# Kernel optimization log

Hardware: AMD Instinct MI355X
Metric: run time of the kernel (lower is better)

The kernel has to match this reference:

```python
import jax, jax.numpy as jnp
import numpy as np

B, S, H = 2, 2048, 2048
NH, NKV, HD = 32, 8, 64
MAXP = 4096


def _apply_rope(x, cos, sin, positions):
    # x: [b, h, s, d]; cos/sin: [max_pos, d//2]; positions: [b, s]
    c = cos[positions][:, None]  # [b,1,s,d/2]
    s_ = sin[positions][:, None]
    x1 = x[..., ::2]
    x2 = x[..., 1::2]
    rotated = jnp.stack((-x2, x1), axis=-1).reshape(x.shape)  # interleave
    c2 = jnp.concatenate([c, c], axis=-1)   # repeat(1,1,1,2) tiling
    s2 = jnp.concatenate([s_, s_], axis=-1)
    return x * c2 + rotated * s2


def setup_inputs() -> dict:
    key = jax.random.key(0)
    ks = jax.random.split(key, 10)
    hidden_states = jax.random.normal(ks[0], (B, S, H), dtype=jnp.float32)
    # RoPE tables (use real rotary tables for realism)
    inv_freq = 1.0 / (10000.0 ** (jnp.arange(0, HD, 2, dtype=jnp.float32) / HD))
    t = jnp.arange(MAXP, dtype=jnp.float32)
    freqs = jnp.outer(t, inv_freq)  # [max_pos, d/2]
    cos = jnp.cos(freqs)
    sin = jnp.sin(freqs)
    positions = jnp.broadcast_to(jnp.arange(S, dtype=jnp.int32), (B, S))
    # additive causal mask
    neg = jnp.finfo(jnp.float32).min
    mask = jnp.where(jnp.tril(jnp.ones((S, S), dtype=bool)), 0.0, neg)[None, None]
    sc = 1.0 / np.sqrt(H)
    q_w = jax.random.normal(ks[1], (NH * HD, H), dtype=jnp.float32) * sc
    q_b = jnp.zeros((NH * HD,), dtype=jnp.float32)
    k_w = jax.random.normal(ks[2], (NKV * HD, H), dtype=jnp.float32) * sc
    k_b = jnp.zeros((NKV * HD,), dtype=jnp.float32)
    v_w = jax.random.normal(ks[3], (NKV * HD, H), dtype=jnp.float32) * sc
    v_b = jnp.zeros((NKV * HD,), dtype=jnp.float32)
    o_w = jax.random.normal(ks[4], (H, NH * HD), dtype=jnp.float32) * sc
    return {"hidden_states": hidden_states, "cos": cos, "sin": sin,
            "positions": positions, "mask": mask,
            "q_w": q_w, "q_b": q_b, "k_w": k_w, "k_b": k_b,
            "v_w": v_w, "v_b": v_b, "o_w": o_w}


def reference(hidden_states, cos, sin, positions, mask, q_w, q_b, k_w, k_b, v_w, v_b, o_w):
    bsz, seq_len, _ = hidden_states.shape
    groups = NH // NKV
    q = (hidden_states @ q_w.T + q_b).reshape(bsz, seq_len, NH, HD).transpose(0, 2, 1, 3)
    k = (hidden_states @ k_w.T + k_b).reshape(bsz, seq_len, NKV, HD).transpose(0, 2, 1, 3)
    v = (hidden_states @ v_w.T + v_b).reshape(bsz, seq_len, NKV, HD).transpose(0, 2, 1, 3)
    q = _apply_rope(q, cos, sin, positions)
    k = _apply_rope(k, cos, sin, positions)
    if groups > 1:
        k = jnp.repeat(k, groups, axis=1)
        v = jnp.repeat(v, groups, axis=1)
    scale = 1.0 / np.sqrt(HD)
    attn = jnp.einsum('bhqd,bhkd->bhqk', q, k) * scale
    attn = attn + mask
    attn = jax.nn.softmax(attn.astype(jnp.float32), axis=-1).astype(q.dtype)
    out = jnp.einsum('bhqk,bhkd->bhqd', attn, v)
    out = out.transpose(0, 2, 1, 3).reshape(bsz, seq_len, NH * HD)
    return out @ o_w.T
```

## Files before the change

kernel.cpp:

```cpp
#include <hip/hip_runtime.h>
#include <hip/hip_bf16.h>

#define BB   2
#define SS   2048
#define HH   2048
#define NH   32
#define NKV  8
#define HD   64
#define NTOK (BB * SS)
#define NQKV (NH * HD + 2 * NKV * HD)
#define KOFF (NH * HD)
#define VOFF (NH * HD + NKV * HD)

#define QSC  0.1803368801111244f

typedef short  short8  __attribute__((ext_vector_type(8)));
typedef short  short4v __attribute__((ext_vector_type(4)));
typedef float  float4v __attribute__((ext_vector_type(4)));

using bf16 = __hip_bfloat16;

#define DEV static __device__ __forceinline__

DEV short8 load8(const bf16* p) { return *(const short8*)p; }
DEV short8 load8s(const short* p) { return *(const short8*)p; }

DEV short f2bfbits(float f) {
    union { bf16 h; short s; } u;
    u.h = __float2bfloat16(f);
    return u.s;
}

DEV unsigned int packbf2(float a, float b) {
    return (unsigned int)(unsigned short)f2bfbits(a)
         | ((unsigned int)(unsigned short)f2bfbits(b) << 16);
}

DEV void async16(const bf16* g, short* l) {
    __builtin_amdgcn_global_load_lds(
        (const __attribute__((address_space(1))) unsigned int*)g,
        (__attribute__((address_space(3))) unsigned int*)l, 16, 0, 0);
}

__global__ __launch_bounds__(256) void cvt_all_kernel(
    const float* __restrict__ hidden, const float* __restrict__ q_w,
    const float* __restrict__ k_w, const float* __restrict__ v_w,
    const float* __restrict__ o_w,
    bf16* __restrict__ Hb, bf16* __restrict__ Wqkv, bf16* __restrict__ Wo) {
    int blk = blockIdx.x;
    const float* src;
    bf16* dst;
    int off;
    if (blk < 8192)       { src = hidden; dst = Hb;   off = blk * 1024; }
    else if (blk < 12288) { src = q_w; dst = Wqkv;    off = (blk - 8192) * 1024; }
    else if (blk < 13312) { src = k_w; dst = Wqkv + (size_t)KOFF * HH; off = (blk - 12288) * 1024; }
    else if (blk < 14336) { src = v_w; dst = Wqkv + (size_t)VOFF * HH; off = (blk - 13312) * 1024; }
    else                  { src = o_w; dst = Wo;      off = (blk - 14336) * 1024; }
    int i = off + threadIdx.x * 4;
    float4 v = *(const float4*)(src + i);
    short4v o;
    o[0] = f2bfbits(v.x); o[1] = f2bfbits(v.y);
    o[2] = f2bfbits(v.z); o[3] = f2bfbits(v.w);
    *(short4v*)(dst + i) = o;
}
#define CVT_BLOCKS 18432

struct GemmCtx {
    const bf16 *gA, *gB;
    short *lA, *lB;
    const short *rdA, *rdB;
    int p0;
};

DEV void gemm_setup(GemmCtx& c, const bf16* A, const bf16* Bw, int K,
                    int m0, int n0, short* As, short* Bs) {
    int lane = threadIdx.x & 63, w = threadIdx.x >> 6;
    int quad = lane >> 4, tq = lane & 15;
    int srow = lane >> 3;
    int schunk = (lane & 7) ^ srow;
    c.gA = A  + (size_t)(m0 + w * 32 + srow) * K + schunk * 8;
    c.gB = Bw + (size_t)(n0 + w * 32 + srow) * K + schunk * 8;
    c.lA = As + (w * 32) * 64;
    c.lB = Bs + (w * 32) * 64;
    int mbase = (w >> 1) * 64, nbase = (w & 1) * 64;
    c.rdA = As + (mbase + tq) * 64;
    c.rdB = Bs + (nbase + tq) * 64;
    c.p0 = (quad ^ (tq & 7)) * 8;
}

DEV void gemm_mainloop(GemmCtx& c, int K, float4v acc[4][4]) {
    for (int k0 = 0; k0 < K; k0 += 64) {
        __syncthreads();
#pragma unroll
        for (int cc = 0; cc < 4; ++cc) {
            async16(c.gA + (size_t)cc * 8 * K + k0, c.lA + cc * 8 * 64);
            async16(c.gB + (size_t)cc * 8 * K + k0, c.lB + cc * 8 * 64);
        }
        __syncthreads();
#pragma unroll
        for (int kh = 0; kh < 2; ++kh) {
            int off = c.p0 ^ (kh * 32);
            short8 af[4], bfr[4];
#pragma unroll
            for (int mi = 0; mi < 4; ++mi) af[mi]  = load8s(c.rdA + mi * 16 * 64 + off);
#pragma unroll
            for (int nj = 0; nj < 4; ++nj) bfr[nj] = load8s(c.rdB + nj * 16 * 64 + off);
#pragma unroll
            for (int mi = 0; mi < 4; ++mi)
#pragma unroll
                for (int nj = 0; nj < 4; ++nj)
                    acc[mi][nj] = __builtin_amdgcn_mfma_f32_16x16x32_bf16(
                        af[mi], bfr[nj], acc[mi][nj], 0, 0, 0);
        }
    }
}

__global__ __launch_bounds__(256, 3) void qkv_kernel(
    const bf16* __restrict__ Hb, const bf16* __restrict__ Wqkv,
    const float* __restrict__ qbias, const float* __restrict__ kbias,
    const float* __restrict__ vbias,
    const float* __restrict__ cosp, const float* __restrict__ sinp,
    const int* __restrict__ posp,
    bf16* __restrict__ Qb, bf16* __restrict__ Kb, bf16* __restrict__ Vt) {
    __shared__ __align__(16) short As[128 * 64];
    __shared__ __align__(16) short Bs[128 * 64];
    int lane = threadIdx.x & 63, w = threadIdx.x >> 6;
    int quad = lane >> 4, tq = lane & 15;
    int flat = blockIdx.x;
    int wg = (flat & 7) * 96 + (flat >> 3);
    int bm = wg / 24, bn = wg % 24;
    int m0 = bm * 128, n0 = bn * 128;
    int mbase = (w >> 1) * 64, nbase = (w & 1) * 64;

    GemmCtx c;
    gemm_setup(c, Hb, Wqkv, HH, m0, n0, As, Bs);
    float4v acc[4][4] = {};
    gemm_mainloop(c, HH, acc);

    float biasv[4];
#pragma unroll
    for (int nj = 0; nj < 4; ++nj) {
        int colg = n0 + nbase + nj * 16 + tq;
        biasv[nj] = (colg < KOFF) ? qbias[colg]
                  : (colg < VOFF) ? kbias[colg - KOFF] : vbias[colg - VOFF];
    }

#pragma unroll
    for (int mi = 0; mi < 4; ++mi) {
#pragma unroll
        for (int r = 0; r < 4; ++r) {
            int tok = m0 + mbase + mi * 16 + quad * 4 + r;
            int p = posp[tok];
#pragma unroll
            for (int nj = 0; nj < 4; ++nj) {
                int colg = n0 + nbase + nj * 16 + tq;
                float val = acc[mi][nj][r] + biasv[nj];
                if (colg < VOFF) {
                    float pv = __shfl_xor(val, 1);
                    int jh = colg & 63;
                    float Cv = cosp[p * 32 + (jh & 31)];
                    float Sv = sinp[p * 32 + (jh & 31)];
                    float outv = (jh & 1) ? (val * Cv + pv * Sv)
                                          : (val * Cv - pv * Sv);
                    if (colg < KOFF)
                        Qb[(size_t)tok * (NH * HD) + colg] = __float2bfloat16(outv * QSC);
                    else
                        Kb[(size_t)tok * (NKV * HD) + (colg - KOFF)] = __float2bfloat16(outv);
                } else {
                    int c2 = colg - VOFF;
                    int kv = c2 >> 6, d = c2 & 63;
                    int bb = tok >> 11, s = tok & (SS - 1);
                    Vt[(((size_t)bb * NKV + kv) * HD + d) * SS + s] = __float2bfloat16(val);
                }
            }
        }
    }
}

__global__ __launch_bounds__(256, 3) void oproj_kernel(
    const bf16* __restrict__ AO, const bf16* __restrict__ Wo,
    float* __restrict__ out) {
    __shared__ __align__(16) short As[128 * 64];
    __shared__ __align__(16) short Bs[128 * 64];
    int lane = threadIdx.x & 63, w = threadIdx.x >> 6;
    int quad = lane >> 4, tq = lane & 15;
    int flat = blockIdx.x;
    int wg = (flat & 7) * 64 + (flat >> 3);
    int bm = wg >> 4, bn = wg & 15;
    int m0 = bm * 128, n0 = bn * 128;
    int mbase = (w >> 1) * 64, nbase = (w & 1) * 64;

    GemmCtx c;
    gemm_setup(c, AO, Wo, NH * HD, m0, n0, As, Bs);
    float4v acc[4][4] = {};
    gemm_mainloop(c, NH * HD, acc);

#pragma unroll
    for (int mi = 0; mi < 4; ++mi) {
#pragma unroll
        for (int nj = 0; nj < 4; ++nj) {
            int colg = n0 + nbase + nj * 16 + tq;
#pragma unroll
            for (int r = 0; r < 4; ++r) {
                int tok = m0 + mbase + mi * 16 + quad * 4 + r;
                out[(size_t)tok * HH + colg] = acc[mi][nj][r];
            }
        }
    }
}

#define PST  72
#define KVSZ (64 * 64)

DEV void attn_stage(int buf, int kv0, int w, int lane,
                    const bf16* __restrict__ Kg, const bf16* __restrict__ Vg,
                    short* Ks, short* Vs) {
    int srow = lane >> 3;
    int schunk = (lane & 7) ^ srow;
#pragma unroll
    for (int cc = 0; cc < 2; ++cc) {
        int rl = w * 16 + cc * 8;
        async16(Kg + (size_t)(kv0 + rl + srow) * (NKV * HD) + schunk * 8,
                Ks + buf * KVSZ + rl * 64);
        async16(Vg + (size_t)(rl + srow) * SS + kv0 + schunk * 8,
                Vs + buf * KVSZ + rl * 64);
    }
}

template<bool MASK>
DEV void attn_compute(int kv0, int qw0, int qw1, int quad, int tq,
                      const short* __restrict__ Ks, const short* __restrict__ Vs,
                      short* myp,
                      const short8 (&aq)[2][2], float4v (&ot)[4][2], float (&ls)[2]) {
    int p0 = (quad ^ (tq & 7)) * 8;

#pragma unroll
    for (int t = 0; t < 4; ++t) {
        const short* kr = Ks + (t * 16 + tq) * 64;
        short8 k0 = load8s(kr + p0);
        short8 k1 = load8s(kr + (p0 ^ 32));
        float4v s0 = {0.f, 0.f, 0.f, 0.f};
        float4v s1 = {0.f, 0.f, 0.f, 0.f};
        s0 = __builtin_amdgcn_mfma_f32_16x16x32_bf16(k0, aq[0][0], s0, 0, 0, 0);
        s0 = __builtin_amdgcn_mfma_f32_16x16x32_bf16(k1, aq[0][1], s0, 0, 0, 0);
        s1 = __builtin_amdgcn_mfma_f32_16x16x32_bf16(k0, aq[1][0], s1, 0, 0, 0);
        s1 = __builtin_amdgcn_mfma_f32_16x16x32_bf16(k1, aq[1][1], s1, 0, 0, 0);
#pragma unroll
        for (int qc = 0; qc < 2; ++qc) {
            const float4v& s = qc ? s1 : s0;
            int qw = qc ? qw1 : qw0;
            float p[4];
#pragma unroll
            for (int r = 0; r < 4; ++r) {
                float e = __builtin_amdgcn_exp2f(s[r]);
                if (MASK) {
                    int kvg = kv0 + t * 16 + quad * 4 + r;
                    e = (kvg <= qw) ? e : 0.f;
                }
                p[r] = e;
                ls[qc] += e;
            }
            int pos = (qc * 16 + tq) * PST + t * 16 + quad * 4;
            *(unsigned int*)(myp + pos)     = packbf2(p[0], p[1]);
            *(unsigned int*)(myp + pos + 2) = packbf2(p[2], p[3]);
        }
    }

    short8 pf00 = load8s(myp + tq * PST + quad * 8);
    short8 pf01 = load8s(myp + tq * PST + 32 + quad * 8);
    short8 pf10 = load8s(myp + (16 + tq) * PST + quad * 8);
    short8 pf11 = load8s(myp + (16 + tq) * PST + 32 + quad * 8);

#pragma unroll
    for (int i = 0; i < 4; ++i) {
        const short* vr = Vs + (i * 16 + tq) * 64;
        short8 bv0 = load8s(vr + p0);
        short8 bv1 = load8s(vr + (p0 ^ 32));
        ot[i][0] = __builtin_amdgcn_mfma_f32_16x16x32_bf16(bv0, pf00, ot[i][0], 0, 0, 0);
        ot[i][0] = __builtin_amdgcn_mfma_f32_16x16x32_bf16(bv1, pf01, ot[i][0], 0, 0, 0);
        ot[i][1] = __builtin_amdgcn_mfma_f32_16x16x32_bf16(bv0, pf10, ot[i][1], 0, 0, 0);
        ot[i][1] = __builtin_amdgcn_mfma_f32_16x16x32_bf16(bv1, pf11, ot[i][1], 0, 0, 0);
    }
}

DEV void attn_superblock(int sb, int b, int h, int w, int lane, int quad, int tq,
                         const bf16* __restrict__ Qb,
                         const bf16* __restrict__ Kg, const bf16* __restrict__ Vg,
                         short* Ks, short* Vs, short* myp, bf16* __restrict__ AO) {
    int qw0 = sb + w * 32 + tq;
    int qw1 = qw0 + 16;
    const bf16* Qr0 = Qb + (size_t)(b * SS + qw0) * (NH * HD) + h * HD + quad * 8;
    const bf16* Qr1 = Qr0 + (size_t)16 * (NH * HD);
    short8 aq[2][2];
    aq[0][0] = load8(Qr0); aq[0][1] = load8(Qr0 + 32);
    aq[1][0] = load8(Qr1); aq[1][1] = load8(Qr1 + 32);

    float4v ot[4][2] = {};
    float ls[2] = {0.f, 0.f};

    const int n = sb / 64 + 2;
    attn_stage(0, 0, w, lane, Kg, Vg, Ks, Vs);

    for (int i = 0; i < n; ++i) {
        int kv0 = i * 64;
        if (i + 1 < n) {
            attn_stage((i + 1) & 1, kv0 + 64, w, lane, Kg, Vg, Ks, Vs);
            asm volatile("s_waitcnt vmcnt(4)" ::: "memory");
        } else {
            asm volatile("s_waitcnt vmcnt(0)" ::: "memory");
        }
        __builtin_amdgcn_s_barrier();
        const short* Kc = Ks + (i & 1) * KVSZ;
        const short* Vc = Vs + (i & 1) * KVSZ;
        if (kv0 < sb)
            attn_compute<false>(kv0, qw0, qw1, quad, tq, Kc, Vc, myp, aq, ot, ls);
        else
            attn_compute<true>(kv0, qw0, qw1, quad, tq, Kc, Vc, myp, aq, ot, ls);
        asm volatile("s_waitcnt lgkmcnt(0)" ::: "memory");
        __builtin_amdgcn_s_barrier();
    }

#pragma unroll
    for (int qc = 0; qc < 2; ++qc) {
        float lsum = ls[qc];
        lsum += __shfl_xor(lsum, 16);
        lsum += __shfl_xor(lsum, 32);
        float inv = 1.0f / lsum;
        int qg = qc ? qw1 : qw0;
        bf16* obase = AO + (size_t)(b * SS + qg) * (NH * HD) + h * HD + quad * 4;
#pragma unroll
        for (int i = 0; i < 4; ++i) {
            short4v o;
#pragma unroll
            for (int r = 0; r < 4; ++r) o[r] = f2bfbits(ot[i][qc][r] * inv);
            *(short4v*)(obase + i * 16) = o;
        }
    }
}

__global__ __launch_bounds__(256, 2) void attn_kernel(
    const bf16* __restrict__ Qb, const bf16* __restrict__ Kb,
    const bf16* __restrict__ Vt, bf16* __restrict__ AO) {
    __shared__ __align__(16) short Ks[2 * KVSZ];
    __shared__ __align__(16) short Vs[2 * KVSZ];
    __shared__ __align__(16) short plds[4][32 * PST];

    int lane = threadIdx.x & 63, w = threadIdx.x >> 6;
    int quad = lane >> 4, tq = lane & 15;

    int x = blockIdx.x;
    int xcd = x & 7, xi = x >> 3;
    int pair = xcd * 2 + (xi & 1);
    int b = pair >> 3, kvh = pair & 7;
    int h = kvh * 4 + (xi >> 1);

    const bf16* Kg = Kb + (size_t)(b * SS) * (NKV * HD) + kvh * HD;
    const bf16* Vg = Vt + (size_t)((b * NKV + kvh) * HD) * SS;
    short* myp = &plds[w][0];

    int jq = blockIdx.y;
    attn_superblock((15 - jq) * 128, b, h, w, lane, quad, tq, Qb, Kg, Vg, Ks, Vs, myp, AO);
    attn_superblock(jq * 128,        b, h, w, lane, quad, tq, Qb, Kg, Vg, Ks, Vs, myp, AO);
}

extern "C" void kernel_launch(void* const* d_in, const int* in_sizes, int n_in,
                              void* d_out, int out_size, void* d_ws, size_t ws_size,
                              hipStream_t stream) {
    const float* hidden = (const float*)d_in[0];
    const float* cosp   = (const float*)d_in[1];
    const float* sinp   = (const float*)d_in[2];
    const int*   posp   = (const int*)d_in[3];
    const float* q_w = (const float*)d_in[5];
    const float* q_b = (const float*)d_in[6];
    const float* k_w = (const float*)d_in[7];
    const float* k_b = (const float*)d_in[8];
    const float* v_w = (const float*)d_in[9];
    const float* v_b = (const float*)d_in[10];
    const float* o_w = (const float*)d_in[11];
    float* out = (float*)d_out;

    char* ws = (char*)d_ws;
    bf16* Hb   = (bf16*)ws; ws += (size_t)NTOK * HH * 2;
    bf16* Wqkv = (bf16*)ws; ws += (size_t)NQKV * HH * 2;
    bf16* Wo   = (bf16*)ws; ws += (size_t)HH * (NH * HD) * 2;
    bf16* Qb   = (bf16*)ws; ws += (size_t)NTOK * (NH * HD) * 2;
    bf16* Kb   = (bf16*)ws; ws += (size_t)NTOK * (NKV * HD) * 2;
    bf16* Vt   = (bf16*)ws; ws += (size_t)NTOK * (NKV * HD) * 2;
    bf16* AO   = (bf16*)ws; ws += (size_t)NTOK * (NH * HD) * 2;

    cvt_all_kernel<<<CVT_BLOCKS, 256, 0, stream>>>(
        hidden, q_w, k_w, v_w, o_w, Hb, Wqkv, Wo);

    qkv_kernel<<<dim3(768), 256, 0, stream>>>(
        Hb, Wqkv, q_b, k_b, v_b, cosp, sinp, posp, Qb, Kb, Vt);

    attn_kernel<<<dim3(64, 8), 256, 0, stream>>>(Qb, Kb, Vt, AO);

    oproj_kernel<<<dim3(512), 256, 0, stream>>>(AO, Wo, out);
}
```

Baseline: 304.6 us.

## Use 256x256 double-buffered ping-pong GEMM for QKV and split attention grid

```diff
diff --git a/kernel.cpp b/kernel.cpp
--- a/kernel.cpp
+++ b/kernel.cpp
@@ -65,95 +65,169 @@
 }
 #define CVT_BLOCKS 18432
 
-struct GemmCtx {
-    const bf16 *gA, *gB;
-    short *lA, *lB;
-    const short *rdA, *rdB;
-    int p0;
-};
-
-DEV void gemm_setup(GemmCtx& c, const bf16* A, const bf16* Bw, int K,
-                    int m0, int n0, short* As, short* Bs) {
-    int lane = threadIdx.x & 63, w = threadIdx.x >> 6;
-    int quad = lane >> 4, tq = lane & 15;
-    int srow = lane >> 3;
-    int schunk = (lane & 7) ^ srow;
-    c.gA = A  + (size_t)(m0 + w * 32 + srow) * K + schunk * 8;
-    c.gB = Bw + (size_t)(n0 + w * 32 + srow) * K + schunk * 8;
-    c.lA = As + (w * 32) * 64;
-    c.lB = Bs + (w * 32) * 64;
-    int mbase = (w >> 1) * 64, nbase = (w & 1) * 64;
-    c.rdA = As + (mbase + tq) * 64;
-    c.rdB = Bs + (nbase + tq) * 64;
-    c.p0 = (quad ^ (tq & 7)) * 8;
-}
-
-DEV void gemm_mainloop(GemmCtx& c, int K, float4v acc[4][4]) {
-    for (int k0 = 0; k0 < K; k0 += 64) {
-        __syncthreads();
-#pragma unroll
-        for (int cc = 0; cc < 4; ++cc) {
-            async16(c.gA + (size_t)cc * 8 * K + k0, c.lA + cc * 8 * 64);
-            async16(c.gB + (size_t)cc * 8 * K + k0, c.lB + cc * 8 * 64);
-        }
-        __syncthreads();
-#pragma unroll
-        for (int kh = 0; kh < 2; ++kh) {
-            int off = c.p0 ^ (kh * 32);
-            short8 af[4], bfr[4];
-#pragma unroll
-            for (int mi = 0; mi < 4; ++mi) af[mi]  = load8s(c.rdA + mi * 16 * 64 + off);
-#pragma unroll
-            for (int nj = 0; nj < 4; ++nj) bfr[nj] = load8s(c.rdB + nj * 16 * 64 + off);
+
+#define STA256(buf, r0, kt) async16(gA + (size_t)(r0) * K + (kt) * 64, lA + (buf) * TSZ + (r0) * 64)
+#define STB256(buf, r0, kt) async16(gB + (size_t)(r0) * K + (kt) * 64, lB + (buf) * TSZ + (r0) * 64)
+
+template<int K>
+DEV void gemm256_loop(const bf16* __restrict__ A, const bf16* __restrict__ Bw,
+                      int m0, int n0, short* sA, short* sB,
+                      float4v (&acc)[8][4]) {
+    constexpr int NT  = K / 64;
+    constexpr int TSZ = 256 * 64;
+
+    const int lane = threadIdx.x & 63, w = threadIdx.x >> 6;
+    const int quad = lane >> 4, tq = lane & 15;
+    const int wm = w >> 2, wn = w & 3;
+    const int srow = lane >> 3;
+    const int schunk = (lane & 7) ^ srow;
+
+    const bf16* gA = A  + (size_t)(m0 + w * 8 + srow) * K + schunk * 8;
+    const bf16* gB = Bw + (size_t)(n0 + w * 8 + srow) * K + schunk * 8;
+    short* lA = sA + w * 8 * 64;
+    short* lB = sB + w * 8 * 64;
+
+    STA256(0, 0, 0); STA256(0, 64, 0); STA256(0, 128, 0); STA256(0, 192, 0);
+    STB256(0, 0, 0); STB256(0, 64, 0); STB256(0, 128, 0); STB256(0, 192, 0);
+    STA256(1, 0, 1); STA256(1, 64, 1); STA256(1, 128, 1); STA256(1, 192, 1);
+    STB256(1, 0, 1); STB256(1, 64, 1); STB256(1, 128, 1); STB256(1, 192, 1);
+    asm volatile("s_waitcnt vmcnt(8)" ::: "memory");
+    __builtin_amdgcn_s_barrier();
+
+    const int p0 = (quad ^ (tq & 7)) * 8;
+
+    for (int t = 0; t < NT; ++t) {
+        const int buf = t & 1;
+        const short* rA = sA + buf * TSZ + (wm * 128 + tq) * 64;
+        const short* rB = sB + buf * TSZ + (wn * 64 + tq) * 64;
+        const bool st = (t + 2 < NT);
+        short8 a03[4][2], a47[4][2], b01[2][2], b23[2][2];
+
+#pragma unroll
+        for (int mi = 0; mi < 4; ++mi) {
+            a03[mi][0] = load8s(rA + mi * 16 * 64 + p0);
+            a03[mi][1] = load8s(rA + mi * 16 * 64 + (p0 ^ 32));
+        }
+#pragma unroll
+        for (int nj = 0; nj < 2; ++nj) {
+            b01[nj][0] = load8s(rB + nj * 16 * 64 + p0);
+            b01[nj][1] = load8s(rB + nj * 16 * 64 + (p0 ^ 32));
+        }
+        __builtin_amdgcn_s_barrier();
+        asm volatile("s_waitcnt lgkmcnt(0)" ::: "memory");
+        __builtin_amdgcn_sched_barrier(0);
+        __builtin_amdgcn_s_setprio(1);
+#pragma unroll
+        for (int kh = 0; kh < 2; ++kh)
 #pragma unroll
             for (int mi = 0; mi < 4; ++mi)
 #pragma unroll
-                for (int nj = 0; nj < 4; ++nj)
-                    acc[mi][nj] = __builtin_amdgcn_mfma_f32_16x16x32_bf16(
-                        af[mi], bfr[nj], acc[mi][nj], 0, 0, 0);
-        }
-    }
-}
-
-__global__ __launch_bounds__(256, 3) void qkv_kernel(
+                for (int nq = 0; nq < 2; ++nq)
+                    acc[mi][nq] = __builtin_amdgcn_mfma_f32_16x16x32_bf16(
+                        a03[mi][kh], b01[nq][kh], acc[mi][nq], 0, 0, 0);
+        __builtin_amdgcn_s_setprio(0);
+        __builtin_amdgcn_s_barrier();
+
+#pragma unroll
+        for (int nj = 0; nj < 2; ++nj) {
+            b23[nj][0] = load8s(rB + (2 + nj) * 16 * 64 + p0);
+            b23[nj][1] = load8s(rB + (2 + nj) * 16 * 64 + (p0 ^ 32));
+        }
+        if (st) { STA256(buf, 0, t + 2); STA256(buf, 128, t + 2); }
+        __builtin_amdgcn_s_barrier();
+        asm volatile("s_waitcnt lgkmcnt(0)" ::: "memory");
+        __builtin_amdgcn_sched_barrier(0);
+        __builtin_amdgcn_s_setprio(1);
+#pragma unroll
+        for (int kh = 0; kh < 2; ++kh)
+#pragma unroll
+            for (int mi = 0; mi < 4; ++mi)
+#pragma unroll
+                for (int nq = 0; nq < 2; ++nq)
+                    acc[mi][2 + nq] = __builtin_amdgcn_mfma_f32_16x16x32_bf16(
+                        a03[mi][kh], b23[nq][kh], acc[mi][2 + nq], 0, 0, 0);
+        __builtin_amdgcn_s_setprio(0);
+        __builtin_amdgcn_s_barrier();
+
+#pragma unroll
+        for (int mi = 0; mi < 4; ++mi) {
+            a47[mi][0] = load8s(rA + (4 + mi) * 16 * 64 + p0);
+            a47[mi][1] = load8s(rA + (4 + mi) * 16 * 64 + (p0 ^ 32));
+        }
+        if (st) { STB256(buf, 0, t + 2);   STB256(buf, 64, t + 2);
+                  STB256(buf, 128, t + 2); STB256(buf, 192, t + 2); }
+        __builtin_amdgcn_s_barrier();
+        asm volatile("s_waitcnt lgkmcnt(0)" ::: "memory");
+        __builtin_amdgcn_sched_barrier(0);
+        __builtin_amdgcn_s_setprio(1);
+#pragma unroll
+        for (int kh = 0; kh < 2; ++kh)
+#pragma unroll
+            for (int mi = 0; mi < 4; ++mi)
+#pragma unroll
+                for (int nq = 0; nq < 2; ++nq)
+                    acc[4 + mi][nq] = __builtin_amdgcn_mfma_f32_16x16x32_bf16(
+                        a47[mi][kh], b01[nq][kh], acc[4 + mi][nq], 0, 0, 0);
+        __builtin_amdgcn_s_setprio(0);
+        __builtin_amdgcn_s_barrier();
+
+        if (st) { STA256(buf, 64, t + 2); STA256(buf, 192, t + 2); }
+        __builtin_amdgcn_s_barrier();
+        __builtin_amdgcn_s_setprio(1);
+#pragma unroll
+        for (int kh = 0; kh < 2; ++kh)
+#pragma unroll
+            for (int mi = 0; mi < 4; ++mi)
+#pragma unroll
+                for (int nq = 0; nq < 2; ++nq)
+                    acc[4 + mi][2 + nq] = __builtin_amdgcn_mfma_f32_16x16x32_bf16(
+                        a47[mi][kh], b23[nq][kh], acc[4 + mi][2 + nq], 0, 0, 0);
+        __builtin_amdgcn_s_setprio(0);
+        if (st) asm volatile("s_waitcnt vmcnt(8)" ::: "memory");
+        else    asm volatile("s_waitcnt vmcnt(0)" ::: "memory");
+        __builtin_amdgcn_s_barrier();
+    }
+}
+
+__global__ __launch_bounds__(512, 2) void qkv8_kernel(
     const bf16* __restrict__ Hb, const bf16* __restrict__ Wqkv,
     const float* __restrict__ qbias, const float* __restrict__ kbias,
     const float* __restrict__ vbias,
     const float* __restrict__ cosp, const float* __restrict__ sinp,
     const int* __restrict__ posp,
     bf16* __restrict__ Qb, bf16* __restrict__ Kb, bf16* __restrict__ Vt) {
-    __shared__ __align__(16) short As[128 * 64];
-    __shared__ __align__(16) short Bs[128 * 64];
+    __shared__ __align__(16) short sA[2 * 256 * 64];
+    __shared__ __align__(16) short sB[2 * 256 * 64];
+
+    int flat = blockIdx.x;
+    int wg = (flat & 7) * 24 + (flat >> 3);
+    int bm = wg / 12, bn = wg % 12;
+    int m0 = bm * 256, n0 = bn * 256;
+
+    float4v acc[8][4] = {};
+    gemm256_loop<HH>(Hb, Wqkv, m0, n0, sA, sB, acc);
+
     int lane = threadIdx.x & 63, w = threadIdx.x >> 6;
     int quad = lane >> 4, tq = lane & 15;
-    int flat = blockIdx.x;
-    int wg = (flat & 7) * 96 + (flat >> 3);
-    int bm = wg / 24, bn = wg % 24;
-    int m0 = bm * 128, n0 = bn * 128;
-    int mbase = (w >> 1) * 64, nbase = (w & 1) * 64;
-
-    GemmCtx c;
-    gemm_setup(c, Hb, Wqkv, HH, m0, n0, As, Bs);
-    float4v acc[4][4] = {};
-    gemm_mainloop(c, HH, acc);
+    int wm = w >> 2, wn = w & 3;
 
     float biasv[4];
 #pragma unroll
     for (int nj = 0; nj < 4; ++nj) {
-        int colg = n0 + nbase + nj * 16 + tq;
+        int colg = n0 + wn * 64 + nj * 16 + tq;
         biasv[nj] = (colg < KOFF) ? qbias[colg]
                   : (colg < VOFF) ? kbias[colg - KOFF] : vbias[colg - VOFF];
     }
 
 #pragma unroll
-    for (int mi = 0; mi < 4; ++mi) {
+    for (int mi = 0; mi < 8; ++mi) {
 #pragma unroll
         for (int r = 0; r < 4; ++r) {
-            int tok = m0 + mbase + mi * 16 + quad * 4 + r;
+            int tok = m0 + wm * 128 + mi * 16 + quad * 4 + r;
             int p = posp[tok];
 #pragma unroll
             for (int nj = 0; nj < 4; ++nj) {
-                int colg = n0 + nbase + nj * 16 + tq;
+                int colg = n0 + wn * 64 + nj * 16 + tq;
                 float val = acc[mi][nj][r] + biasv[nj];
                 if (colg < VOFF) {
                     float pv = __shfl_xor(val, 1);
@@ -177,6 +251,56 @@
     }
 }
 
+struct GemmCtx {
+    const bf16 *gA, *gB;
+    short *lA, *lB;
+    const short *rdA, *rdB;
+    int p0;
+};
+
+DEV void gemm_setup(GemmCtx& c, const bf16* A, const bf16* Bw, int K,
+                    int m0, int n0, short* As, short* Bs) {
+    int lane = threadIdx.x & 63, w = threadIdx.x >> 6;
+    int quad = lane >> 4, tq = lane & 15;
+    int srow = lane >> 3;
+    int schunk = (lane & 7) ^ srow;
+    c.gA = A  + (size_t)(m0 + w * 32 + srow) * K + schunk * 8;
+    c.gB = Bw + (size_t)(n0 + w * 32 + srow) * K + schunk * 8;
+    c.lA = As + (w * 32) * 64;
+    c.lB = Bs + (w * 32) * 64;
+    int mbase = (w >> 1) * 64, nbase = (w & 1) * 64;
+    c.rdA = As + (mbase + tq) * 64;
+    c.rdB = Bs + (nbase + tq) * 64;
+    c.p0 = (quad ^ (tq & 7)) * 8;
+}
+
+DEV void gemm_mainloop(GemmCtx& c, int K, float4v acc[4][4]) {
+    for (int k0 = 0; k0 < K; k0 += 64) {
+        __syncthreads();
+#pragma unroll
+        for (int cc = 0; cc < 4; ++cc) {
+            async16(c.gA + (size_t)cc * 8 * K + k0, c.lA + cc * 8 * 64);
+            async16(c.gB + (size_t)cc * 8 * K + k0, c.lB + cc * 8 * 64);
+        }
+        __syncthreads();
+#pragma unroll
+        for (int kh = 0; kh < 2; ++kh) {
+            int off = c.p0 ^ (kh * 32);
+            short8 af[4], bfr[4];
+#pragma unroll
+            for (int mi = 0; mi < 4; ++mi) af[mi]  = load8s(c.rdA + mi * 16 * 64 + off);
+#pragma unroll
+            for (int nj = 0; nj < 4; ++nj) bfr[nj] = load8s(c.rdB + nj * 16 * 64 + off);
+#pragma unroll
+            for (int mi = 0; mi < 4; ++mi)
+#pragma unroll
+                for (int nj = 0; nj < 4; ++nj)
+                    acc[mi][nj] = __builtin_amdgcn_mfma_f32_16x16x32_bf16(
+                        af[mi], bfr[nj], acc[mi][nj], 0, 0, 0);
+        }
+    }
+}
+
 __global__ __launch_bounds__(256, 3) void oproj_kernel(
     const bf16* __restrict__ AO, const bf16* __restrict__ Wo,
     float* __restrict__ out) {
@@ -241,10 +365,12 @@
         short8 k1 = load8s(kr + (p0 ^ 32));
         float4v s0 = {0.f, 0.f, 0.f, 0.f};
         float4v s1 = {0.f, 0.f, 0.f, 0.f};
+        __builtin_amdgcn_s_setprio(1);
         s0 = __builtin_amdgcn_mfma_f32_16x16x32_bf16(k0, aq[0][0], s0, 0, 0, 0);
         s0 = __builtin_amdgcn_mfma_f32_16x16x32_bf16(k1, aq[0][1], s0, 0, 0, 0);
         s1 = __builtin_amdgcn_mfma_f32_16x16x32_bf16(k0, aq[1][0], s1, 0, 0, 0);
         s1 = __builtin_amdgcn_mfma_f32_16x16x32_bf16(k1, aq[1][1], s1, 0, 0, 0);
+        __builtin_amdgcn_s_setprio(0);
 #pragma unroll
         for (int qc = 0; qc < 2; ++qc) {
             const float4v& s = qc ? s1 : s0;
@@ -276,10 +402,12 @@
         const short* vr = Vs + (i * 16 + tq) * 64;
         short8 bv0 = load8s(vr + p0);
         short8 bv1 = load8s(vr + (p0 ^ 32));
+        __builtin_amdgcn_s_setprio(1);
         ot[i][0] = __builtin_amdgcn_mfma_f32_16x16x32_bf16(bv0, pf00, ot[i][0], 0, 0, 0);
         ot[i][0] = __builtin_amdgcn_mfma_f32_16x16x32_bf16(bv1, pf01, ot[i][0], 0, 0, 0);
         ot[i][1] = __builtin_amdgcn_mfma_f32_16x16x32_bf16(bv0, pf10, ot[i][1], 0, 0, 0);
         ot[i][1] = __builtin_amdgcn_mfma_f32_16x16x32_bf16(bv1, pf11, ot[i][1], 0, 0, 0);
+        __builtin_amdgcn_s_setprio(0);
     }
 }
 
@@ -338,7 +466,7 @@
     }
 }
 
-__global__ __launch_bounds__(256, 2) void attn_kernel(
+__global__ __launch_bounds__(256, 3) void attn_kernel(
     const bf16* __restrict__ Qb, const bf16* __restrict__ Kb,
     const bf16* __restrict__ Vt, bf16* __restrict__ AO) {
     __shared__ __align__(16) short Ks[2 * KVSZ];
@@ -358,9 +486,8 @@
     const bf16* Vg = Vt + (size_t)((b * NKV + kvh) * HD) * SS;
     short* myp = &plds[w][0];
 
-    int jq = blockIdx.y;
-    attn_superblock((15 - jq) * 128, b, h, w, lane, quad, tq, Qb, Kg, Vg, Ks, Vs, myp, AO);
-    attn_superblock(jq * 128,        b, h, w, lane, quad, tq, Qb, Kg, Vg, Ks, Vs, myp, AO);
+    int sb = (15 - (int)blockIdx.y) * 128;
+    attn_superblock(sb, b, h, w, lane, quad, tq, Qb, Kg, Vg, Ks, Vs, myp, AO);
 }
 
 extern "C" void kernel_launch(void* const* d_in, const int* in_sizes, int n_in,
@@ -391,10 +518,10 @@
     cvt_all_kernel<<<CVT_BLOCKS, 256, 0, stream>>>(
         hidden, q_w, k_w, v_w, o_w, Hb, Wqkv, Wo);
 
-    qkv_kernel<<<dim3(768), 256, 0, stream>>>(
+    qkv8_kernel<<<dim3(192), 512, 0, stream>>>(
         Hb, Wqkv, q_b, k_b, v_b, cosp, sinp, posp, Qb, Kb, Vt);
 
-    attn_kernel<<<dim3(64, 8), 256, 0, stream>>>(Qb, Kb, Vt, AO);
+    attn_kernel<<<dim3(64, 16), 256, 0, stream>>>(Qb, Kb, Vt, AO);
 
     oproj_kernel<<<dim3(512), 256, 0, stream>>>(AO, Wo, out);
 }
```

After: 324.3 us. 1.06x slower.
